# Kernel optimization log

Measured on AMD Instinct MI355X. Metric: run time of the kernel, lower is better.

The kernel has to match this reference:

```python
import jax, jax.numpy as jnp
import numpy as np

B, S, D, C, WD, I = 8, 14, 2048, 20, 300, 1024  # batch, imgSize, imgFeatureDim, classNum, wordFeatureDim, intermediaDim


def setup_inputs() -> dict:
    key = jax.random.key(0)
    ks = jax.random.split(key, 8)
    s = 0.02
    return {
        "imgFeaturemap": jax.random.normal(ks[0], (B, S, S, D), jnp.float32),
        "wordFeatures": jax.random.normal(ks[1], (C, WD), jnp.float32),
        "W1": jax.random.normal(ks[2], (I, D), jnp.float32) * s,   # fc1, no bias
        "W2": jax.random.normal(ks[3], (I, WD), jnp.float32) * s,  # fc2, no bias
        "W3": jax.random.normal(ks[4], (I, I), jnp.float32) * s,   # fc3
        "b3": jax.random.normal(ks[5], (I,), jnp.float32) * s,
        "W4": jax.random.normal(ks[6], (1, I), jnp.float32) * s,   # fc4
        "b4": jax.random.normal(ks[7], (1,), jnp.float32) * s,
    }


def reference(imgFeaturemap, wordFeatures, W1, W2, W3, b3, W4, b4):
    b, s, _, d = imgFeaturemap.shape
    c = wordFeatures.shape[0]
    n = b * s * s  # number of spatial locations across batch

    h_img = imgFeaturemap.reshape(n, d) @ W1.T          # [N, I]
    h_word = wordFeatures @ W2.T                         # [C, I]
    # broadcasted elementwise product + tanh (original materializes via repeat)
    t = jnp.tanh(h_img[:, None, :] * h_word[None, :, :])  # [N, C, I]
    feat = t @ W3.T + b3                                  # [N, C, I]
    coef = (feat @ W4.T)[..., 0] + b4[0]                  # [N, C]
    # softmax over spatial positions per (batch, class)
    coef = jax.nn.softmax(coef.reshape(b, s * s, c), axis=1).reshape(b, s, s, c)
    # weighted feature map and class-wise pooled semantic features
    fmwc = imgFeaturemap[:, :, :, None, :] * coef[..., None]  # [B, S, S, C, D]
    semanticFeature = fmwc.sum(axis=(1, 2))                    # [B, C, D]
    return semanticFeature, fmwc, coef
```

## Files before the change

### kernel.cpp

```cpp
#include <hip/hip_runtime.h>

typedef __attribute__((ext_vector_type(4))) float float4_t;
typedef __attribute__((ext_vector_type(8))) short short8_t;
typedef __attribute__((ext_vector_type(4))) unsigned short ushort4_t;

#define B_ 8
#define S_ 14
#define P_ 196
#define N_ 1568
#define D_ 2048
#define C_ 20
#define WD_ 300
#define I_ 1024
#define PS_ 14

__device__ __forceinline__ unsigned short f2bf(float f) {
    unsigned u = __builtin_bit_cast(unsigned, f);
    u += 0x7FFFu + ((u >> 16) & 1u);
    return (unsigned short)(u >> 16);
}

__global__ void cvt_all_kernel(const float* __restrict__ img, const float* __restrict__ W1,
                               unsigned short* __restrict__ Xb, unsigned short* __restrict__ W1b) {
    int bid = blockIdx.x;
    const float* src;
    unsigned short* dst;
    int i4;
    if (bid < 3136) { i4 = bid * 256 + threadIdx.x; src = img; dst = Xb; }
    else            { i4 = (bid - 3136) * 256 + threadIdx.x; src = W1; dst = W1b; }
    float4_t v = ((const float4_t*)src)[i4];
    ushort4_t o;
    o.x = f2bf(v.x); o.y = f2bf(v.y); o.z = f2bf(v.z); o.w = f2bf(v.w);
    ((ushort4_t*)dst)[i4] = o;
}

__global__ __launch_bounds__(256) void prep_kernel(const float* __restrict__ wf,
                                                   const float* __restrict__ W2,
                                                   const float* __restrict__ W3,
                                                   const float* __restrict__ b3,
                                                   const float* __restrict__ W4,
                                                   const float* __restrict__ b4,
                                                   float* __restrict__ hw,
                                                   float* __restrict__ we,
                                                   float* __restrict__ bias) {
    int bid = blockIdx.x, tid = threadIdx.x;
    if (bid < 80) {
        int idx = bid * 256 + tid;
        int c = idx >> 10, i = idx & 1023;
        const float* wr  = wf + c * WD_;
        const float* w2r = W2 + i * WD_;
        float s = 0.f;
        #pragma unroll 4
        for (int k = 0; k < WD_; k++) s += wr[k] * w2r[k];
        hw[idx] = s;
    } else if (bid < 96) {
        __shared__ float red[256];
        int blk = bid - 80;
        int i0 = blk * 64;
        int q = tid >> 6, col = tid & 63;
        float s = 0.f;
        #pragma unroll 4
        for (int j = q * 256; j < q * 256 + 256; j++)
            s += W4[j] * W3[j * I_ + i0 + col];
        red[tid] = s;
        __syncthreads();
        if (tid < 64)
            we[i0 + tid] = red[tid] + red[tid + 64] + red[tid + 128] + red[tid + 192];
    } else {
        __shared__ float r[256];
        float s = 0.f;
        for (int j = tid; j < I_; j += 256) s += b3[j] * W4[j];
        r[tid] = s;
        __syncthreads();
        for (int o = 128; o > 0; o >>= 1) {
            if (tid < o) r[tid] += r[tid + o];
            __syncthreads();
        }
        if (tid == 0) bias[0] = r[0] + b4[0];
    }
}

__global__ __launch_bounds__(256) void gemm_himg_kernel(const unsigned short* __restrict__ Xb,
                                                        const unsigned short* __restrict__ W1b,
                                                        float* __restrict__ H) {
    int wave = blockIdx.x * 4 + (threadIdx.x >> 6);
    int lane = threadIdx.x & 63;
    int mjob = wave >> 4;
    int njob = wave & 15;
    int m0 = mjob * 32, n0 = njob * 64;
    int ra = lane & 15;
    int kq = (lane >> 4) * 8;

    float4_t acc[2][4] = {};
    const unsigned short* xa = Xb  + (size_t)(m0 + ra) * D_ + kq;
    const unsigned short* wb = W1b + (size_t)(n0 + ra) * D_ + kq;

    #pragma unroll 2
    for (int k0 = 0; k0 < D_; k0 += 32) {
        short8_t a0 = *(const short8_t*)(xa + k0);
        short8_t a1 = *(const short8_t*)(xa + 16 * D_ + k0);
        short8_t b0 = *(const short8_t*)(wb + k0);
        short8_t b1 = *(const short8_t*)(wb + 16 * D_ + k0);
        short8_t b2 = *(const short8_t*)(wb + 32 * D_ + k0);
        short8_t b3v = *(const short8_t*)(wb + 48 * D_ + k0);
        acc[0][0] = __builtin_amdgcn_mfma_f32_16x16x32_bf16(a0, b0, acc[0][0], 0, 0, 0);
        acc[0][1] = __builtin_amdgcn_mfma_f32_16x16x32_bf16(a0, b1, acc[0][1], 0, 0, 0);
        acc[0][2] = __builtin_amdgcn_mfma_f32_16x16x32_bf16(a0, b2, acc[0][2], 0, 0, 0);
        acc[0][3] = __builtin_amdgcn_mfma_f32_16x16x32_bf16(a0, b3v, acc[0][3], 0, 0, 0);
        acc[1][0] = __builtin_amdgcn_mfma_f32_16x16x32_bf16(a1, b0, acc[1][0], 0, 0, 0);
        acc[1][1] = __builtin_amdgcn_mfma_f32_16x16x32_bf16(a1, b1, acc[1][1], 0, 0, 0);
        acc[1][2] = __builtin_amdgcn_mfma_f32_16x16x32_bf16(a1, b2, acc[1][2], 0, 0, 0);
        acc[1][3] = __builtin_amdgcn_mfma_f32_16x16x32_bf16(a1, b3v, acc[1][3], 0, 0, 0);
    }

    int col = lane & 15, rq = (lane >> 4) * 4;
    #pragma unroll
    for (int mt = 0; mt < 2; mt++) {
        #pragma unroll
        for (int nt = 0; nt < 4; nt++) {
            float4_t v = acc[mt][nt];
            int rbase = m0 + mt * 16 + rq;
            int cidx = n0 + nt * 16 + col;
            H[(rbase + 0) * I_ + cidx] = v.x;
            H[(rbase + 1) * I_ + cidx] = v.y;
            H[(rbase + 2) * I_ + cidx] = v.z;
            H[(rbase + 3) * I_ + cidx] = v.w;
        }
    }
}

__global__ __launch_bounds__(256) void logits_kernel(const float* __restrict__ H,
                                                     const float* __restrict__ hw,
                                                     const float* __restrict__ we,
                                                     const float* __restrict__ bias,
                                                     float* __restrict__ lg) {
    __shared__ float sh[4][I_];
    __shared__ float sw[I_];
    int n0 = blockIdx.x * 4, tid = threadIdx.x;
    #pragma unroll
    for (int t = 0; t < 4; t++) {
        int idx = tid + 256 * t;
        sw[idx] = we[idx];
        #pragma unroll
        for (int nn = 0; nn < 4; nn++)
            sh[nn][idx] = H[(size_t)(n0 + nn) * I_ + idx];
    }
    __syncthreads();
    int wv = tid >> 6, lane = tid & 63;
    float bz = bias[0];
    for (int j = 0; j < 5; j++) {
        int c = j * 4 + wv;
        const float* hwc = hw + c * I_;
        float a0 = 0.f, a1 = 0.f, a2 = 0.f, a3 = 0.f;
        #pragma unroll 2
        for (int i = lane; i < I_; i += 64) {
            float hv = hwc[i], wvv = sw[i];
            float x0 = sh[0][i] * hv;
            float x1 = sh[1][i] * hv;
            float x2 = sh[2][i] * hv;
            float x3 = sh[3][i] * hv;
            float t0 = 1.f - __fdividef(2.f, __expf(2.f * x0) + 1.f);
            float t1 = 1.f - __fdividef(2.f, __expf(2.f * x1) + 1.f);
            float t2 = 1.f - __fdividef(2.f, __expf(2.f * x2) + 1.f);
            float t3 = 1.f - __fdividef(2.f, __expf(2.f * x3) + 1.f);
            a0 += t0 * wvv; a1 += t1 * wvv; a2 += t2 * wvv; a3 += t3 * wvv;
        }
        #pragma unroll
        for (int o = 32; o > 0; o >>= 1) {
            a0 += __shfl_down(a0, o);
            a1 += __shfl_down(a1, o);
            a2 += __shfl_down(a2, o);
            a3 += __shfl_down(a3, o);
        }
        if (lane == 0) {
            lg[(n0 + 0) * C_ + c] = a0 + bz;
            lg[(n0 + 1) * C_ + c] = a1 + bz;
            lg[(n0 + 2) * C_ + c] = a2 + bz;
            lg[(n0 + 3) * C_ + c] = a3 + bz;
        }
    }
}

__global__ __launch_bounds__(256) void softmax_kernel(const float* __restrict__ lg,
                                                      float* __restrict__ coef) {
    __shared__ float r[4];
    __shared__ float bval;
    int bx = blockIdx.x;
    int b = bx / C_, c = bx % C_;
    int tid = threadIdx.x, wv = tid >> 6, lane = tid & 63;
    float v = (tid < P_) ? lg[(b * P_ + tid) * C_ + c] : -3.0e38f;
    float m = v;
    #pragma unroll
    for (int o = 32; o > 0; o >>= 1) m = fmaxf(m, __shfl_down(m, o));
    if (lane == 0) r[wv] = m;
    __syncthreads();
    if (tid == 0) bval = fmaxf(fmaxf(r[0], r[1]), fmaxf(r[2], r[3]));
    __syncthreads();
    float mx = bval;
    float e = (tid < P_) ? __expf(v - mx) : 0.f;
    float s = e;
    #pragma unroll
    for (int o = 32; o > 0; o >>= 1) s += __shfl_down(s, o);
    __syncthreads();
    if (lane == 0) r[wv] = s;
    __syncthreads();
    if (tid == 0) bval = r[0] + r[1] + r[2] + r[3];
    __syncthreads();
    if (tid < P_) coef[(b * P_ + tid) * C_ + c] = e / bval;
}

__global__ __launch_bounds__(256) void fmwc_kernel(const float* __restrict__ img,
                                                   const float* __restrict__ coef,
                                                   float* __restrict__ fm) {
    __shared__ float sc[C_];
    int bp = blockIdx.x, tid = threadIdx.x;
    if (tid < C_) sc[tid] = coef[bp * C_ + tid];
    __syncthreads();
    const float4_t* ir = (const float4_t*)(img + (size_t)bp * D_);
    float4_t v0 = ir[tid], v1 = ir[tid + 256];
    float4_t* ob = (float4_t*)(fm + (size_t)bp * C_ * D_);
    #pragma unroll
    for (int c = 0; c < C_; c++) {
        float s = sc[c];
        ob[c * 512 + tid] = v0 * s;
        ob[c * 512 + tid + 256] = v1 * s;
    }
}

__global__ __launch_bounds__(256) void semantic_part_kernel(const float* __restrict__ img,
                                                            const float* __restrict__ coef,
                                                            float* __restrict__ part) {
    __shared__ float sc[PS_ * C_];
    int bx = blockIdx.x;
    int ps = bx >> 4;
    int b = (bx >> 1) & 7;
    int ch = bx & 1;
    int tid = threadIdx.x;
    for (int q = tid; q < PS_ * C_; q += 256)
        sc[q] = coef[(b * P_ + ps * PS_) * C_ + q];
    __syncthreads();
    const float4_t* base = (const float4_t*)(img + (size_t)(b * P_ + ps * PS_) * D_ + ch * 1024) + tid;
    float4_t acc[C_];
    #pragma unroll
    for (int c = 0; c < C_; c++) acc[c] = (float4_t){0.f, 0.f, 0.f, 0.f};
    for (int pp = 0; pp < PS_; pp++) {
        float4_t v = base[pp * 512];
        #pragma unroll
        for (int c = 0; c < C_; c++) acc[c] += v * sc[pp * C_ + c];
    }
    float* pb = part + ((size_t)(ps * B_ + b) * C_) * D_ + ch * 1024 + tid * 4;
    #pragma unroll
    for (int c = 0; c < C_; c++) *(float4_t*)(pb + c * D_) = acc[c];
}

__global__ __launch_bounds__(256) void semantic_reduce_kernel(const float* __restrict__ part,
                                                              float* __restrict__ sem) {
    int idx = blockIdx.x * 256 + threadIdx.x;
    const float4_t* p4 = (const float4_t*)part;
    float4_t s = {0.f, 0.f, 0.f, 0.f};
    #pragma unroll
    for (int ps = 0; ps < PS_; ps++) s += p4[(size_t)ps * 81920 + idx];
    ((float4_t*)sem)[idx] = s;
}

extern "C" void kernel_launch(void* const* d_in, const int* in_sizes, int n_in,
                              void* d_out, int out_size, void* d_ws, size_t ws_size,
                              hipStream_t stream) {
    const float* img = (const float*)d_in[0];
    const float* wf  = (const float*)d_in[1];
    const float* W1  = (const float*)d_in[2];
    const float* W2  = (const float*)d_in[3];
    const float* W3  = (const float*)d_in[4];
    const float* b3  = (const float*)d_in[5];
    const float* W4  = (const float*)d_in[6];
    const float* b4  = (const float*)d_in[7];

    float* out  = (float*)d_out;
    float* sem  = out;
    float* fm   = out + (size_t)B_ * C_ * D_;
    float* coef = fm + (size_t)N_ * C_ * D_;

    char* ws = (char*)d_ws;
    unsigned short* Xb  = (unsigned short*)ws;
    unsigned short* W1b = (unsigned short*)(ws + 6422528);
    float* H    = (float*)(ws + 10616832);
    float* hw   = (float*)(ws + 17039360);
    float* we   = (float*)(ws + 17121280);
    float* bias = (float*)(ws + 17125376);
    float* lg   = (float*)(ws + 17125632);
    float* part = (float*)(ws + 17251072);

    cvt_all_kernel<<<5184, 256, 0, stream>>>(img, W1, Xb, W1b);
    prep_kernel<<<97, 256, 0, stream>>>(wf, W2, W3, b3, W4, b4, hw, we, bias);
    gemm_himg_kernel<<<196, 256, 0, stream>>>(Xb, W1b, H);
    logits_kernel<<<N_ / 4, 256, 0, stream>>>(H, hw, we, bias, lg);
    softmax_kernel<<<B_ * C_, 256, 0, stream>>>(lg, coef);
    semantic_part_kernel<<<PS_ * B_ * 2, 256, 0, stream>>>(img, coef, part);
    semantic_reduce_kernel<<<320, 256, 0, stream>>>(part, sem);
    fmwc_kernel<<<N_, 256, 0, stream>>>(img, coef, fm);
}
```

Measured before the change: 414.1 us.

## Fuse conversion with prep, shrink GEMM tiles, fuse fmwc writes into semantic pass

Merges the bf16 conversion and the small prep work into one launch. Halves the GEMM wave tile width from 64 to 32 columns so twice as many blocks run. Folds the weighted feature-map store into the semantic partial-sum kernel, so the image is read once for both outputs instead of twice. The fused kernel uses only 448 blocks of 128 threads to write the large fmwc output, which may underfill the GPU and limit write bandwidth compared with the old 1568-block fmwc kernel.

Result: slower. 441.2 us (+6.6%).

```diff
diff --git a/kernel.cpp b/kernel.cpp
--- a/kernel.cpp
+++ b/kernel.cpp
@@ -20,32 +20,35 @@
     return (unsigned short)(u >> 16);
 }
 
-__global__ void cvt_all_kernel(const float* __restrict__ img, const float* __restrict__ W1,
-                               unsigned short* __restrict__ Xb, unsigned short* __restrict__ W1b) {
-    int bid = blockIdx.x;
-    const float* src;
-    unsigned short* dst;
-    int i4;
-    if (bid < 3136) { i4 = bid * 256 + threadIdx.x; src = img; dst = Xb; }
-    else            { i4 = (bid - 3136) * 256 + threadIdx.x; src = W1; dst = W1b; }
-    float4_t v = ((const float4_t*)src)[i4];
-    ushort4_t o;
-    o.x = f2bf(v.x); o.y = f2bf(v.y); o.z = f2bf(v.z); o.w = f2bf(v.w);
-    ((ushort4_t*)dst)[i4] = o;
-}
-
-__global__ __launch_bounds__(256) void prep_kernel(const float* __restrict__ wf,
-                                                   const float* __restrict__ W2,
-                                                   const float* __restrict__ W3,
-                                                   const float* __restrict__ b3,
-                                                   const float* __restrict__ W4,
-                                                   const float* __restrict__ b4,
-                                                   float* __restrict__ hw,
-                                                   float* __restrict__ we,
-                                                   float* __restrict__ bias) {
+__global__ __launch_bounds__(256) void cvt_prep_kernel(const float* __restrict__ img,
+                                                       const float* __restrict__ W1,
+                                                       unsigned short* __restrict__ Xb,
+                                                       unsigned short* __restrict__ W1b,
+                                                       const float* __restrict__ wf,
+                                                       const float* __restrict__ W2,
+                                                       const float* __restrict__ W3,
+                                                       const float* __restrict__ b3,
+                                                       const float* __restrict__ W4,
+                                                       const float* __restrict__ b4,
+                                                       float* __restrict__ hw,
+                                                       float* __restrict__ we,
+                                                       float* __restrict__ bias) {
     int bid = blockIdx.x, tid = threadIdx.x;
-    if (bid < 80) {
-        int idx = bid * 256 + tid;
+    if (bid < 5184) {
+        const float* src;
+        unsigned short* dst;
+        int i4;
+        if (bid < 3136) { i4 = bid * 256 + tid; src = img; dst = Xb; }
+        else            { i4 = (bid - 3136) * 256 + tid; src = W1; dst = W1b; }
+        float4_t v = ((const float4_t*)src)[i4];
+        ushort4_t o;
+        o.x = f2bf(v.x); o.y = f2bf(v.y); o.z = f2bf(v.z); o.w = f2bf(v.w);
+        ((ushort4_t*)dst)[i4] = o;
+        return;
+    }
+    int pb = bid - 5184;
+    if (pb < 80) {
+        int idx = pb * 256 + tid;
         int c = idx >> 10, i = idx & 1023;
         const float* wr  = wf + c * WD_;
         const float* w2r = W2 + i * WD_;
@@ -53,9 +56,9 @@
         #pragma unroll 4
         for (int k = 0; k < WD_; k++) s += wr[k] * w2r[k];
         hw[idx] = s;
-    } else if (bid < 96) {
+    } else if (pb < 96) {
         __shared__ float red[256];
-        int blk = bid - 80;
+        int blk = pb - 80;
         int i0 = blk * 64;
         int q = tid >> 6, col = tid & 63;
         float s = 0.f;
@@ -85,13 +88,13 @@
                                                         float* __restrict__ H) {
     int wave = blockIdx.x * 4 + (threadIdx.x >> 6);
     int lane = threadIdx.x & 63;
-    int mjob = wave >> 4;
-    int njob = wave & 15;
-    int m0 = mjob * 32, n0 = njob * 64;
+    int mjob = wave >> 5;
+    int njob = wave & 31;
+    int m0 = mjob * 32, n0 = njob * 32;
     int ra = lane & 15;
     int kq = (lane >> 4) * 8;
 
-    float4_t acc[2][4] = {};
+    float4_t acc[2][2] = {};
     const unsigned short* xa = Xb  + (size_t)(m0 + ra) * D_ + kq;
     const unsigned short* wb = W1b + (size_t)(n0 + ra) * D_ + kq;
 
@@ -101,23 +104,17 @@
         short8_t a1 = *(const short8_t*)(xa + 16 * D_ + k0);
         short8_t b0 = *(const short8_t*)(wb + k0);
         short8_t b1 = *(const short8_t*)(wb + 16 * D_ + k0);
-        short8_t b2 = *(const short8_t*)(wb + 32 * D_ + k0);
-        short8_t b3v = *(const short8_t*)(wb + 48 * D_ + k0);
         acc[0][0] = __builtin_amdgcn_mfma_f32_16x16x32_bf16(a0, b0, acc[0][0], 0, 0, 0);
         acc[0][1] = __builtin_amdgcn_mfma_f32_16x16x32_bf16(a0, b1, acc[0][1], 0, 0, 0);
-        acc[0][2] = __builtin_amdgcn_mfma_f32_16x16x32_bf16(a0, b2, acc[0][2], 0, 0, 0);
-        acc[0][3] = __builtin_amdgcn_mfma_f32_16x16x32_bf16(a0, b3v, acc[0][3], 0, 0, 0);
         acc[1][0] = __builtin_amdgcn_mfma_f32_16x16x32_bf16(a1, b0, acc[1][0], 0, 0, 0);
         acc[1][1] = __builtin_amdgcn_mfma_f32_16x16x32_bf16(a1, b1, acc[1][1], 0, 0, 0);
-        acc[1][2] = __builtin_amdgcn_mfma_f32_16x16x32_bf16(a1, b2, acc[1][2], 0, 0, 0);
-        acc[1][3] = __builtin_amdgcn_mfma_f32_16x16x32_bf16(a1, b3v, acc[1][3], 0, 0, 0);
     }
 
     int col = lane & 15, rq = (lane >> 4) * 4;
     #pragma unroll
     for (int mt = 0; mt < 2; mt++) {
         #pragma unroll
-        for (int nt = 0; nt < 4; nt++) {
+        for (int nt = 0; nt < 2; nt++) {
             float4_t v = acc[mt][nt];
             int rbase = m0 + mt * 16 + rq;
             int cidx = n0 + nt * 16 + col;
@@ -209,48 +206,36 @@
     if (tid < P_) coef[(b * P_ + tid) * C_ + c] = e / bval;
 }
 
-__global__ __launch_bounds__(256) void fmwc_kernel(const float* __restrict__ img,
-                                                   const float* __restrict__ coef,
-                                                   float* __restrict__ fm) {
-    __shared__ float sc[C_];
-    int bp = blockIdx.x, tid = threadIdx.x;
-    if (tid < C_) sc[tid] = coef[bp * C_ + tid];
-    __syncthreads();
-    const float4_t* ir = (const float4_t*)(img + (size_t)bp * D_);
-    float4_t v0 = ir[tid], v1 = ir[tid + 256];
-    float4_t* ob = (float4_t*)(fm + (size_t)bp * C_ * D_);
-    #pragma unroll
-    for (int c = 0; c < C_; c++) {
-        float s = sc[c];
-        ob[c * 512 + tid] = v0 * s;
-        ob[c * 512 + tid + 256] = v1 * s;
-    }
-}
-
-__global__ __launch_bounds__(256) void semantic_part_kernel(const float* __restrict__ img,
-                                                            const float* __restrict__ coef,
-                                                            float* __restrict__ part) {
+__global__ __launch_bounds__(128) void fmwc_sem_kernel(const float* __restrict__ img,
+                                                       const float* __restrict__ coef,
+                                                       float* __restrict__ fm,
+                                                       float* __restrict__ part) {
     __shared__ float sc[PS_ * C_];
     int bx = blockIdx.x;
-    int ps = bx >> 4;
-    int b = (bx >> 1) & 7;
-    int ch = bx & 1;
+    int ps = bx >> 5;
+    int b  = (bx >> 2) & 7;
+    int q  = bx & 3;
     int tid = threadIdx.x;
-    for (int q = tid; q < PS_ * C_; q += 256)
-        sc[q] = coef[(b * P_ + ps * PS_) * C_ + q];
-    __syncthreads();
-    const float4_t* base = (const float4_t*)(img + (size_t)(b * P_ + ps * PS_) * D_ + ch * 1024) + tid;
+    for (int t = tid; t < PS_ * C_; t += 128)
+        sc[t] = coef[(b * P_ + ps * PS_) * C_ + t];
+    __syncthreads();
+    const float4_t* base = (const float4_t*)(img + (size_t)(b * P_ + ps * PS_) * D_ + q * 512) + tid;
     float4_t acc[C_];
     #pragma unroll
     for (int c = 0; c < C_; c++) acc[c] = (float4_t){0.f, 0.f, 0.f, 0.f};
     for (int pp = 0; pp < PS_; pp++) {
         float4_t v = base[pp * 512];
-        #pragma unroll
-        for (int c = 0; c < C_; c++) acc[c] += v * sc[pp * C_ + c];
-    }
-    float* pb = part + ((size_t)(ps * B_ + b) * C_) * D_ + ch * 1024 + tid * 4;
-    #pragma unroll
-    for (int c = 0; c < C_; c++) *(float4_t*)(pb + c * D_) = acc[c];
+        float4_t* ob = (float4_t*)(fm + ((size_t)(b * P_ + ps * PS_ + pp) * C_) * D_ + q * 512) + tid;
+        #pragma unroll
+        for (int c = 0; c < C_; c++) {
+            float4_t w = v * sc[pp * C_ + c];
+            ob[c * 512] = w;
+            acc[c] += w;
+        }
+    }
+    float* pbase = part + ((size_t)(ps * B_ + b) * C_) * D_ + q * 512 + tid * 4;
+    #pragma unroll
+    for (int c = 0; c < C_; c++) *(float4_t*)(pbase + c * D_) = acc[c];
 }
 
 __global__ __launch_bounds__(256) void semantic_reduce_kernel(const float* __restrict__ part,
@@ -290,12 +275,10 @@
     float* lg   = (float*)(ws + 17125632);
     float* part = (float*)(ws + 17251072);
 
-    cvt_all_kernel<<<5184, 256, 0, stream>>>(img, W1, Xb, W1b);
-    prep_kernel<<<97, 256, 0, stream>>>(wf, W2, W3, b3, W4, b4, hw, we, bias);
-    gemm_himg_kernel<<<196, 256, 0, stream>>>(Xb, W1b, H);
+    cvt_prep_kernel<<<5281, 256, 0, stream>>>(img, W1, Xb, W1b, wf, W2, W3, b3, W4, b4, hw, we, bias);
+    gemm_himg_kernel<<<392, 256, 0, stream>>>(Xb, W1b, H);
     logits_kernel<<<N_ / 4, 256, 0, stream>>>(H, hw, we, bias, lg);
     softmax_kernel<<<B_ * C_, 256, 0, stream>>>(lg, coef);
-    semantic_part_kernel<<<PS_ * B_ * 2, 256, 0, stream>>>(img, coef, part);
+    fmwc_sem_kernel<<<448, 128, 0, stream>>>(img, coef, fm, part);
     semantic_reduce_kernel<<<320, 256, 0, stream>>>(part, sem);
-    fmwc_kernel<<<N_, 256, 0, stream>>>(img, coef, fm);
-}
+}
```

## Split H_img GEMM over K into two halves and merge cvt/prep kernels

Applied to the files above, without the earlier changes.

Merges the bf16 conversion kernel and the small prep kernel into a single launch, saving one kernel launch. The img@W1 GEMM is split-K into two halves with twice as many blocks (392 instead of 196), so more CUs are busy on the 256-CU device. Each half writes its own partial H buffer, and the logits kernel sums the two partials while loading them. This adds an extra H-sized workspace buffer and more global write and read traffic.

After: 427.6 us. 3.3% more time.

```diff
diff --git a/kernel.cpp b/kernel.cpp
--- a/kernel.cpp
+++ b/kernel.cpp
@@ -20,32 +20,35 @@
     return (unsigned short)(u >> 16);
 }
 
-__global__ void cvt_all_kernel(const float* __restrict__ img, const float* __restrict__ W1,
-                               unsigned short* __restrict__ Xb, unsigned short* __restrict__ W1b) {
-    int bid = blockIdx.x;
-    const float* src;
-    unsigned short* dst;
-    int i4;
-    if (bid < 3136) { i4 = bid * 256 + threadIdx.x; src = img; dst = Xb; }
-    else            { i4 = (bid - 3136) * 256 + threadIdx.x; src = W1; dst = W1b; }
-    float4_t v = ((const float4_t*)src)[i4];
-    ushort4_t o;
-    o.x = f2bf(v.x); o.y = f2bf(v.y); o.z = f2bf(v.z); o.w = f2bf(v.w);
-    ((ushort4_t*)dst)[i4] = o;
-}
-
-__global__ __launch_bounds__(256) void prep_kernel(const float* __restrict__ wf,
-                                                   const float* __restrict__ W2,
-                                                   const float* __restrict__ W3,
-                                                   const float* __restrict__ b3,
-                                                   const float* __restrict__ W4,
-                                                   const float* __restrict__ b4,
-                                                   float* __restrict__ hw,
-                                                   float* __restrict__ we,
-                                                   float* __restrict__ bias) {
+__global__ __launch_bounds__(256) void cvt_prep_kernel(const float* __restrict__ img,
+                                                       const float* __restrict__ W1,
+                                                       unsigned short* __restrict__ Xb,
+                                                       unsigned short* __restrict__ W1b,
+                                                       const float* __restrict__ wf,
+                                                       const float* __restrict__ W2,
+                                                       const float* __restrict__ W3,
+                                                       const float* __restrict__ b3,
+                                                       const float* __restrict__ W4,
+                                                       const float* __restrict__ b4,
+                                                       float* __restrict__ hw,
+                                                       float* __restrict__ we,
+                                                       float* __restrict__ bias) {
     int bid = blockIdx.x, tid = threadIdx.x;
-    if (bid < 80) {
-        int idx = bid * 256 + tid;
+    if (bid < 5184) {
+        const float* src;
+        unsigned short* dst;
+        int i4;
+        if (bid < 3136) { i4 = bid * 256 + tid; src = img; dst = Xb; }
+        else            { i4 = (bid - 3136) * 256 + tid; src = W1; dst = W1b; }
+        float4_t v = ((const float4_t*)src)[i4];
+        ushort4_t o;
+        o.x = f2bf(v.x); o.y = f2bf(v.y); o.z = f2bf(v.z); o.w = f2bf(v.w);
+        ((ushort4_t*)dst)[i4] = o;
+        return;
+    }
+    int pb = bid - 5184;
+    if (pb < 80) {
+        int idx = pb * 256 + tid;
         int c = idx >> 10, i = idx & 1023;
         const float* wr  = wf + c * WD_;
         const float* w2r = W2 + i * WD_;
@@ -53,9 +56,9 @@
         #pragma unroll 4
         for (int k = 0; k < WD_; k++) s += wr[k] * w2r[k];
         hw[idx] = s;
-    } else if (bid < 96) {
+    } else if (pb < 96) {
         __shared__ float red[256];
-        int blk = bid - 80;
+        int blk = pb - 80;
         int i0 = blk * 64;
         int q = tid >> 6, col = tid & 63;
         float s = 0.f;
@@ -85,18 +88,21 @@
                                                         float* __restrict__ H) {
     int wave = blockIdx.x * 4 + (threadIdx.x >> 6);
     int lane = threadIdx.x & 63;
+    int kjob = 0;
+    if (wave >= 784) { kjob = 1; wave -= 784; }
     int mjob = wave >> 4;
     int njob = wave & 15;
     int m0 = mjob * 32, n0 = njob * 64;
     int ra = lane & 15;
     int kq = (lane >> 4) * 8;
+    int kbase = kjob * 1024;
 
     float4_t acc[2][4] = {};
-    const unsigned short* xa = Xb  + (size_t)(m0 + ra) * D_ + kq;
-    const unsigned short* wb = W1b + (size_t)(n0 + ra) * D_ + kq;
+    const unsigned short* xa = Xb  + (size_t)(m0 + ra) * D_ + kbase + kq;
+    const unsigned short* wb = W1b + (size_t)(n0 + ra) * D_ + kbase + kq;
 
     #pragma unroll 2
-    for (int k0 = 0; k0 < D_; k0 += 32) {
+    for (int k0 = 0; k0 < 1024; k0 += 32) {
         short8_t a0 = *(const short8_t*)(xa + k0);
         short8_t a1 = *(const short8_t*)(xa + 16 * D_ + k0);
         short8_t b0 = *(const short8_t*)(wb + k0);
@@ -114,6 +120,7 @@
     }
 
     int col = lane & 15, rq = (lane >> 4) * 4;
+    float* Hk = H + (size_t)kjob * N_ * I_;
     #pragma unroll
     for (int mt = 0; mt < 2; mt++) {
         #pragma unroll
@@ -121,10 +128,10 @@
             float4_t v = acc[mt][nt];
             int rbase = m0 + mt * 16 + rq;
             int cidx = n0 + nt * 16 + col;
-            H[(rbase + 0) * I_ + cidx] = v.x;
-            H[(rbase + 1) * I_ + cidx] = v.y;
-            H[(rbase + 2) * I_ + cidx] = v.z;
-            H[(rbase + 3) * I_ + cidx] = v.w;
+            Hk[(rbase + 0) * I_ + cidx] = v.x;
+            Hk[(rbase + 1) * I_ + cidx] = v.y;
+            Hk[(rbase + 2) * I_ + cidx] = v.z;
+            Hk[(rbase + 3) * I_ + cidx] = v.w;
         }
     }
 }
@@ -143,7 +150,8 @@
         sw[idx] = we[idx];
         #pragma unroll
         for (int nn = 0; nn < 4; nn++)
-            sh[nn][idx] = H[(size_t)(n0 + nn) * I_ + idx];
+            sh[nn][idx] = H[(size_t)(n0 + nn) * I_ + idx]
+                        + H[(size_t)(N_ + n0 + nn) * I_ + idx];
     }
     __syncthreads();
     int wv = tid >> 6, lane = tid & 63;
@@ -284,15 +292,14 @@
     unsigned short* Xb  = (unsigned short*)ws;
     unsigned short* W1b = (unsigned short*)(ws + 6422528);
     float* H    = (float*)(ws + 10616832);
-    float* hw   = (float*)(ws + 17039360);
-    float* we   = (float*)(ws + 17121280);
-    float* bias = (float*)(ws + 17125376);
-    float* lg   = (float*)(ws + 17125632);
-    float* part = (float*)(ws + 17251072);
-
-    cvt_all_kernel<<<5184, 256, 0, stream>>>(img, W1, Xb, W1b);
-    prep_kernel<<<97, 256, 0, stream>>>(wf, W2, W3, b3, W4, b4, hw, we, bias);
-    gemm_himg_kernel<<<196, 256, 0, stream>>>(Xb, W1b, H);
+    float* hw   = (float*)(ws + 23461888);
+    float* we   = (float*)(ws + 23543808);
+    float* bias = (float*)(ws + 23547904);
+    float* lg   = (float*)(ws + 23548160);
+    float* part = (float*)(ws + 23673600);
+
+    cvt_prep_kernel<<<5281, 256, 0, stream>>>(img, W1, Xb, W1b, wf, W2, W3, b3, W4, b4, hw, we, bias);
+    gemm_himg_kernel<<<392, 256, 0, stream>>>(Xb, W1b, H);
     logits_kernel<<<N_ / 4, 256, 0, stream>>>(H, hw, we, bias, lg);
     softmax_kernel<<<B_ * C_, 256, 0, stream>>>(lg, coef);
     semantic_part_kernel<<<PS_ * B_ * 2, 256, 0, stream>>>(img, coef, part);
```
